# Optimization experiments

Measured on AMD Instinct MI355X. Metric: run time of the kernel, lower is better.

## Reference

```python
import jax, jax.numpy as jnp
import numpy as np

B, N, C, H = 4, 1024, 256, 8
HD = C // H
SCALE = HD ** -0.5


def setup_inputs() -> dict:
    key = jax.random.key(0)
    ks = jax.random.split(key, 8)
    x = jax.random.normal(ks[0], (B, N, C), jnp.float32)
    voxel_coord = jax.random.uniform(ks[1], (B, N, 3), jnp.float32)
    # Linear weights stored as [in, out] so y = x @ W + b (same math as torch x @ W.T)
    W_qk = jax.random.normal(ks[2], (C, 2 * C), jnp.float32) * 0.02
    W_v = jax.random.normal(ks[3], (C, C), jnp.float32) * 0.02
    W_proj = jax.random.normal(ks[4], (C, C), jnp.float32) * 0.02
    b_proj = jnp.zeros((C,), jnp.float32)
    W_pos = jax.random.normal(ks[5], (4, H), jnp.float32) * 0.02
    b_pos = jnp.zeros((H,), jnp.float32)
    gating = jnp.ones((H,), jnp.float32)
    return dict(x=x, voxel_coord=voxel_coord, W_qk=W_qk, W_v=W_v,
                W_proj=W_proj, b_proj=b_proj, W_pos=W_pos, b_pos=b_pos,
                gating=gating)


def reference(x, voxel_coord, W_qk, W_v, W_proj, b_proj, W_pos, b_pos, gating):
    b, n, c = x.shape
    # Relative 3D positional encoding: positions[b,i,j] = p[j] - p[i]; feature = [dx,dy,dz,dist]
    diff = voxel_coord[:, None, :, :] - voxel_coord[:, :, None, :]          # [B,N,N,3]
    dist = jnp.sqrt(jnp.sum(diff * diff, axis=-1, keepdims=True))           # [B,N,N,1]
    rel = jnp.concatenate([diff, dist], axis=-1)                            # [B,N,N,4]

    # Positional score per head, softmax over keys j
    pos_logits = jnp.einsum('bijf,fh->bhij', rel, W_pos) + b_pos[None, :, None, None]
    pos_score = jax.nn.softmax(pos_logits, axis=-1)                         # [B,H,N,N]

    # Content score: SDPA with V = I  ==  plain softmax attention matrix
    qk = (x @ W_qk).reshape(b, n, 2, H, HD)
    q = jnp.transpose(qk[:, :, 0], (0, 2, 1, 3))                            # [B,H,N,hd]
    k = jnp.transpose(qk[:, :, 1], (0, 2, 1, 3))
    patch_score = jax.nn.softmax(jnp.einsum('bhid,bhjd->bhij', q, k) * SCALE, axis=-1)

    # Gated mix + renormalize
    sig = jax.nn.sigmoid(gating)[None, :, None, None]
    attn = (1.0 - sig) * patch_score + sig * pos_score
    attn = attn / jnp.sum(attn, axis=-1, keepdims=True)

    v = (x @ W_v).reshape(b, n, H, HD).transpose(0, 2, 1, 3)                # [B,H,N,hd]
    out = jnp.einsum('bhij,bhjd->bihd', attn, v).reshape(b, n, c)           # [B,N,C]
    out = out @ W_proj + b_proj
    return out
```

## Files before the change

### kernel.cpp

```cpp
#include <hip/hip_runtime.h>
#include <hip/hip_bf16.h>

#define LOG2E 1.4426950408889634f

typedef __attribute__((ext_vector_type(8))) short bf16x8_t;
typedef __attribute__((ext_vector_type(4))) float f32x4_t;

#if __has_builtin(__builtin_amdgcn_exp2f)
#define EXP2F_(x) __builtin_amdgcn_exp2f(x)
#else
__device__ __forceinline__ float EXP2F_(float x) {
    float r; asm volatile("v_exp_f32 %0, %1\ns_nop 1" : "=v"(r) : "v"(x)); return r;
}
#endif
#if __has_builtin(__builtin_amdgcn_sqrtf)
#define SQRTF_(x) __builtin_amdgcn_sqrtf(x)
#else
__device__ __forceinline__ float SQRTF_(float x) {
    float r; asm volatile("v_sqrt_f32 %0, %1\ns_nop 1" : "=v"(r) : "v"(x)); return r;
}
#endif

__device__ __forceinline__ unsigned short f2bf(float f) {
    unsigned u = __float_as_uint(f);
    u += 0x7fffu + ((u >> 16) & 1u);
    return (unsigned short)(u >> 16);
}

__device__ __forceinline__ unsigned pk2(float lo, float hi) {
    union { __hip_bfloat162 h2; unsigned u; } cvt;
    cvt.h2 = __float22bfloat162_rn(make_float2(lo, hi));
    return cvt.u;
}

__device__ __forceinline__ void stage16(const unsigned short* g, unsigned short* l, int lane) {
#if __has_builtin(__builtin_amdgcn_global_load_lds)
    __builtin_amdgcn_global_load_lds((const __attribute__((address_space(1))) void*)g,
                                     (__attribute__((address_space(3))) void*)l, 16, 0, 0);
#else
    *(uint4*)((char*)l + lane * 16) = *(const uint4*)g;
#endif
}

__global__ __launch_bounds__(256) void k_convert(
    const float* __restrict__ x, const float* __restrict__ Wqk,
    const float* __restrict__ Wv, const float* __restrict__ Wpj,
    unsigned short* __restrict__ x_bf, unsigned short* __restrict__ Wqk_t,
    unsigned short* __restrict__ Wv_t, unsigned short* __restrict__ Wp_t)
{
    __shared__ unsigned short T[64 * 72];
    const int bid = blockIdx.x, tid = threadIdx.x;
    if (bid < 64) {
        const float* src; unsigned short* dst; int N_, kt, nt;
        if (bid < 32)      { src = Wqk; dst = Wqk_t; N_ = 512; kt = bid & 3; nt = bid >> 2; }
        else if (bid < 48) { int t = bid - 32; src = Wv;  dst = Wv_t; N_ = 256; kt = t & 3; nt = t >> 2; }
        else               { int t = bid - 48; src = Wpj; dst = Wp_t; N_ = 256; kt = t & 3; nt = t >> 2; }
        const int kr = tid >> 2, seg = tid & 3;
        #pragma unroll
        for (int u = 0; u < 4; ++u) {
            float4 v = *(const float4*)(src + (kt * 64 + kr) * N_ + nt * 64 + seg * 16 + u * 4);
            T[(seg * 16 + u * 4 + 0) * 72 + kr] = f2bf(v.x);
            T[(seg * 16 + u * 4 + 1) * 72 + kr] = f2bf(v.y);
            T[(seg * 16 + u * 4 + 2) * 72 + kr] = f2bf(v.z);
            T[(seg * 16 + u * 4 + 3) * 72 + kr] = f2bf(v.w);
        }
        __syncthreads();
        const int n = tid >> 2, s2 = tid & 3;
        uint4 a = *(uint4*)&T[n * 72 + s2 * 16];
        uint4 b2 = *(uint4*)&T[n * 72 + s2 * 16 + 8];
        *(uint4*)(dst + (nt * 64 + n) * 256 + kt * 64 + s2 * 16) = a;
        *(uint4*)(dst + (nt * 64 + n) * 256 + kt * 64 + s2 * 16 + 8) = b2;
    } else {
        const int cb2 = bid - 64;
        const float4* xs = (const float4*)x + (size_t)cb2 * 8192;
        uint2* xd = (uint2*)x_bf + (size_t)cb2 * 8192;
        for (int i = tid; i < 8192; i += 256) {
            float4 v = xs[i];
            uint2 o;
            o.x = (unsigned)f2bf(v.x) | ((unsigned)f2bf(v.y) << 16);
            o.y = (unsigned)f2bf(v.z) | ((unsigned)f2bf(v.w) << 16);
            xd[i] = o;
        }
    }
}

__global__ __launch_bounds__(256) void k_qkv(
    const unsigned short* __restrict__ x_bf,
    const unsigned short* __restrict__ Wqk_t,
    const unsigned short* __restrict__ Wv_t,
    unsigned short* __restrict__ q_ws, unsigned short* __restrict__ k_ws,
    unsigned short* __restrict__ v_ws)
{
    __shared__ unsigned short Al[64 * 64];
    __shared__ unsigned short Bl[64 * 64];
    const int tid = threadIdx.x;
    const int n0 = blockIdx.x * 64;
    const int row0 = blockIdx.y * 64;
    const int w = tid >> 6, lane = tid & 63;
    const int lhi = lane >> 4, llo = lane & 15;
    const unsigned short* Bsrc = (n0 < 512) ? (Wqk_t + n0 * 256) : (Wv_t + (n0 - 512) * 256);

    const int sr = lane >> 3, sc = lane & 7;
    const int scx = sc ^ (sr & 7);

    f32x4_t acc[4] = {};
    for (int kc = 0; kc < 4; ++kc) {
        #pragma unroll
        for (int s = 0; s < 2; ++s) {
            int chunk = w * 2 + s;
            int r = chunk * 8 + sr;
            stage16(x_bf + (row0 + r) * 256 + kc * 64 + scx * 8, &Al[chunk * 512], lane);
            stage16(Bsrc + r * 256 + kc * 64 + scx * 8, &Bl[chunk * 512], lane);
        }
        __syncthreads();
        #pragma unroll
        for (int ks = 0; ks < 2; ++ks) {
            int ua = ((ks * 4 + lhi) ^ (llo & 7)) * 8;
            bf16x8_t a = *(const bf16x8_t*)(&Al[(w * 16 + llo) * 64 + ua]);
            #pragma unroll
            for (int nt = 0; nt < 4; ++nt) {
                bf16x8_t b = *(const bf16x8_t*)(&Bl[(nt * 16 + llo) * 64 + ua]);
                acc[nt] = __builtin_amdgcn_mfma_f32_16x16x32_bf16(a, b, acc[nt], 0, 0, 0);
            }
        }
        __syncthreads();
    }
    constexpr float QSC = (float)(1.4426950408889634 / 5.656854249492380195206754896838);
    #pragma unroll
    for (int nt = 0; nt < 4; ++nt) {
        int ng = n0 + nt * 16 + llo;
        #pragma unroll
        for (int r = 0; r < 4; ++r) {
            int ig = row0 + w * 16 + lhi * 4 + r;
            float val = acc[nt][r];
            int b = ig >> 10, i = ig & 1023;
            if (ng < 256) {
                int h = ng >> 5, d = ng & 31;
                q_ws[((b * 8 + h) * 1024 + i) * 32 + d] = f2bf(val * QSC);
            } else if (ng < 512) {
                int c = ng - 256, h = c >> 5, d = c & 31;
                k_ws[((b * 8 + h) * 1024 + i) * 32 + d] = f2bf(val);
            } else {
                int c = ng - 512, h = c >> 5, d = c & 31;
                v_ws[((b * 8 + h) * 1024 + i) * 32 + d] = f2bf(val);
            }
        }
    }
}

__global__ __launch_bounds__(256) void k_attn(
    const unsigned short* __restrict__ q_ws,
    const unsigned short* __restrict__ k_ws,
    const unsigned short* __restrict__ v_ws,
    const float* __restrict__ coords,
    const float* __restrict__ W_pos,
    const float* __restrict__ b_pos,
    float* __restrict__ part)
{
    __shared__ unsigned short Kl[64 * 32];
    __shared__ unsigned short Vt[32 * 72];
    __shared__ unsigned short Wp[64 * 72];
    __shared__ unsigned short Wq[64 * 72];
    __shared__ float4 XYZS[512];
    __shared__ float  AJ[512];

    const int tid = threadIdx.x;
    const int bid = blockIdx.x;
    const int xcd = bid & 7, idx = bid >> 3;
    const int bh = xcd * 4 + (idx >> 5);
    const int rem = idx & 31;
    const int it = rem >> 1;
    const int jh = rem & 1;
    const int b = bh >> 3, h = bh & 7;

    const int w = tid >> 6, lane = tid & 63;
    const int lhi = lane >> 4, llo = lane & 15;

    const float wxl = W_pos[0 * 8 + h] * LOG2E;
    const float wyl = W_pos[1 * 8 + h] * LOG2E;
    const float wzl = W_pos[2 * 8 + h] * LOG2E;
    const float wdl = W_pos[3 * 8 + h] * LOG2E;
    const float bpl = b_pos[h] * LOG2E;

    const int i_base = it * 64 + w * 16;
    bf16x8_t qf = *(const bf16x8_t*)(q_ws + (bh * 1024 + i_base + llo) * 32 + lhi * 8);

    const float* cb_ = coords + b * 3072;
    const int ig = i_base + llo;
    float xi = cb_[ig * 3 + 0], yi = cb_[ig * 3 + 1], zi = cb_[ig * 3 + 2];
    float si = fmaf(xi, xi, fmaf(yi, yi, zi * zi));
    float cil = fmaf(wzl, zi, fmaf(wyl, yi, wxl * xi));

    for (int jl = tid; jl < 512; jl += 256) {
        int jg = jh * 512 + jl;
        float xj = cb_[jg * 3 + 0], yj = cb_[jg * 3 + 1], zj = cb_[jg * 3 + 2];
        XYZS[jl] = make_float4(xj, yj, zj, fmaf(xj, xj, fmaf(yj, yj, zj * zj)));
        AJ[jl] = fmaf(wzl, zj, fmaf(wyl, yj, wxl * xj)) + bpl;
    }

    bf16x8_t ones;
    #pragma unroll
    for (int e = 0; e < 8; ++e) ones[e] = (short)0x3F80;

    f32x4_t accP[2] = {}, accQ[2] = {};
    f32x4_t accLp = {}, accLq = {};

    const int ksr = lane >> 2, ksc = lane & 3;
    const int kscx = ksc ^ (ksr & 3);
    __syncthreads();

    for (int t = 0; t < 8; ++t) {
        const int j0 = jh * 512 + t * 64;
        const int jlb0 = t * 64;
        {
            int r = w * 16 + ksr;
            stage16(k_ws + (bh * 1024 + j0 + r) * 32 + kscx * 8, &Kl[w * 512], lane);
            uint4 vv = *(const uint4*)(v_ws + (bh * 1024 + j0 + lane) * 32 + w * 8);
            const unsigned short* pv = (const unsigned short*)&vv;
            #pragma unroll
            for (int e = 0; e < 8; ++e) Vt[(w * 8 + e) * 72 + lane] = pv[e];
        }
        __syncthreads();

        #pragma unroll
        for (int jq = 0; jq < 4; ++jq) {
            int krow = jq * 16 + llo;
            bf16x8_t kf = *(const bf16x8_t*)(&Kl[krow * 32 + ((lhi ^ (krow & 3)) * 8)]);
            f32x4_t zero = {};
            f32x4_t sv = __builtin_amdgcn_mfma_f32_16x16x32_bf16(kf, qf, zero, 0, 0, 0);
            int jlb = jlb0 + jq * 16 + lhi * 4;
            float ep[4], eq[4];
            #pragma unroll
            for (int r = 0; r < 4; ++r) {
                float4 cj = XYZS[jlb + r];
                float aj = AJ[jlb + r];
                float dot = fmaf(cj.x, xi, fmaf(cj.y, yi, cj.z * zi));
                float d2 = fmaf(-2.0f, dot, si + cj.w);
                float dist = SQRTF_(d2);
                float spos = fmaf(wdl, dist, aj - cil);
                ep[r] = EXP2F_(sv[r]);
                eq[r] = EXP2F_(spos);
            }
            uint2 wpP, wpQ;
            wpP.x = pk2(ep[0], ep[1]); wpP.y = pk2(ep[2], ep[3]);
            wpQ.x = pk2(eq[0], eq[1]); wpQ.y = pk2(eq[2], eq[3]);
            int off = (w * 16 + llo) * 72 + jq * 16 + lhi * 4;
            *(uint2*)(&Wp[off]) = wpP;
            *(uint2*)(&Wq[off]) = wpQ;
        }

        #pragma unroll
        for (int jb = 0; jb < 2; ++jb) {
            bf16x8_t bP = *(const bf16x8_t*)(&Wp[(w * 16 + llo) * 72 + jb * 32 + lhi * 8]);
            bf16x8_t bQ = *(const bf16x8_t*)(&Wq[(w * 16 + llo) * 72 + jb * 32 + lhi * 8]);
            accLp = __builtin_amdgcn_mfma_f32_16x16x32_bf16(ones, bP, accLp, 0, 0, 0);
            accLq = __builtin_amdgcn_mfma_f32_16x16x32_bf16(ones, bQ, accLq, 0, 0, 0);
            #pragma unroll
            for (int dt = 0; dt < 2; ++dt) {
                bf16x8_t af = *(const bf16x8_t*)(&Vt[(dt * 16 + llo) * 72 + jb * 32 + lhi * 8]);
                accP[dt] = __builtin_amdgcn_mfma_f32_16x16x32_bf16(af, bP, accP[dt], 0, 0, 0);
                accQ[dt] = __builtin_amdgcn_mfma_f32_16x16x32_bf16(af, bQ, accQ[dt], 0, 0, 0);
            }
        }
        __syncthreads();
    }

    float* pb = part + (size_t)((bh * 16 + it) * 2 + jh) * 4224;
    #pragma unroll
    for (int dt = 0; dt < 2; ++dt) {
        #pragma unroll
        for (int r = 0; r < 4; ++r) {
            int d = dt * 16 + lhi * 4 + r;
            pb[d * 64 + w * 16 + llo] = accP[dt][r];
            pb[2048 + d * 64 + w * 16 + llo] = accQ[dt][r];
        }
    }
    if (lane < 16) {
        pb[4096 + w * 16 + lane] = accLp[0];
        pb[4160 + w * 16 + lane] = accLq[0];
    }
}

__global__ __launch_bounds__(256) void k_comb(
    const float* __restrict__ part, const float* __restrict__ gating,
    unsigned short* __restrict__ o_ws)
{
    const int bid = blockIdx.x;
    const int bh = bid >> 4, it = bid & 15;
    const int b = bh >> 3, h = bh & 7;
    const int tid = threadIdx.x, w = tid >> 6, i = tid & 63;
    const float* p0 = part + (size_t)(bid * 2) * 4224;
    const float* p1 = p0 + 4224;
    float sig = 1.0f / (1.0f + __expf(-gating[h]));
    float Lp = p0[4096 + i] + p1[4096 + i];
    float Lq = p0[4160 + i] + p1[4160 + i];
    float ca = (1.0f - sig) / Lp, cb2 = sig / Lq;
    unsigned short ob[8];
    #pragma unroll
    for (int e = 0; e < 8; ++e) {
        int d = w * 8 + e;
        float Op = p0[d * 64 + i] + p1[d * 64 + i];
        float Oq = p0[2048 + d * 64 + i] + p1[2048 + d * 64 + i];
        ob[e] = f2bf(ca * Op + cb2 * Oq);
    }
    *(uint4*)(o_ws + ((size_t)(b * 1024 + it * 64 + i)) * 256 + h * 32 + w * 8) = *(uint4*)ob;
}

__global__ __launch_bounds__(256) void k_proj(
    const unsigned short* __restrict__ A,
    const unsigned short* __restrict__ Bt,
    const float* __restrict__ bias,
    float* __restrict__ out)
{
    __shared__ unsigned short Al[64 * 64];
    __shared__ unsigned short Bl[64 * 64];
    const int tid = threadIdx.x;
    const int n0 = blockIdx.x * 64;
    const int row0 = blockIdx.y * 64;
    const int w = tid >> 6, lane = tid & 63;
    const int lhi = lane >> 4, llo = lane & 15;
    const int sr = lane >> 3, sc = lane & 7;
    const int scx = sc ^ (sr & 7);

    f32x4_t acc[4] = {};
    for (int kc = 0; kc < 4; ++kc) {
        #pragma unroll
        for (int s = 0; s < 2; ++s) {
            int chunk = w * 2 + s;
            int r = chunk * 8 + sr;
            stage16(A + (row0 + r) * 256 + kc * 64 + scx * 8, &Al[chunk * 512], lane);
            stage16(Bt + (n0 + r) * 256 + kc * 64 + scx * 8, &Bl[chunk * 512], lane);
        }
        __syncthreads();
        #pragma unroll
        for (int ks = 0; ks < 2; ++ks) {
            int ua = ((ks * 4 + lhi) ^ (llo & 7)) * 8;
            bf16x8_t a = *(const bf16x8_t*)(&Al[(w * 16 + llo) * 64 + ua]);
            #pragma unroll
            for (int nt = 0; nt < 4; ++nt) {
                bf16x8_t b = *(const bf16x8_t*)(&Bl[(nt * 16 + llo) * 64 + ua]);
                acc[nt] = __builtin_amdgcn_mfma_f32_16x16x32_bf16(a, b, acc[nt], 0, 0, 0);
            }
        }
        __syncthreads();
    }
    #pragma unroll
    for (int nt = 0; nt < 4; ++nt) {
        int ng = n0 + nt * 16 + llo;
        float bv = bias[ng];
        #pragma unroll
        for (int r = 0; r < 4; ++r) {
            int ig = row0 + w * 16 + lhi * 4 + r;
            out[ig * 256 + ng] = acc[nt][r] + bv;
        }
    }
}

extern "C" void kernel_launch(void* const* d_in, const int* in_sizes, int n_in,
                              void* d_out, int out_size, void* d_ws, size_t ws_size,
                              hipStream_t stream)
{
    const float* x    = (const float*)d_in[0];
    const float* vc   = (const float*)d_in[1];
    const float* Wqk  = (const float*)d_in[2];
    const float* Wv   = (const float*)d_in[3];
    const float* Wpj  = (const float*)d_in[4];
    const float* bpj  = (const float*)d_in[5];
    const float* Wpos = (const float*)d_in[6];
    const float* bpos = (const float*)d_in[7];
    const float* gat  = (const float*)d_in[8];
    float* out = (float*)d_out;

    char* ws = (char*)d_ws;
    unsigned short* x_bf  = (unsigned short*)(ws + 0);
    unsigned short* Wqk_t = (unsigned short*)(ws + 2097152);
    unsigned short* Wv_t  = (unsigned short*)(ws + 2359296);
    unsigned short* Wp_t  = (unsigned short*)(ws + 2490368);
    unsigned short* q_ws  = (unsigned short*)(ws + 2621440);
    unsigned short* k_ws  = (unsigned short*)(ws + 4718592);
    unsigned short* v_ws  = (unsigned short*)(ws + 6815744);
    unsigned short* o_ws  = (unsigned short*)(ws + 8912896);
    float*          partf = (float*)(ws + 11010048);

    hipLaunchKernelGGL(k_convert, dim3(96), dim3(256), 0, stream,
                       x, Wqk, Wv, Wpj, x_bf, Wqk_t, Wv_t, Wp_t);
    hipLaunchKernelGGL(k_qkv, dim3(12, 64), dim3(256), 0, stream,
                       x_bf, Wqk_t, Wv_t, q_ws, k_ws, v_ws);
    hipLaunchKernelGGL(k_attn, dim3(1024), dim3(256), 0, stream,
                       q_ws, k_ws, v_ws, vc, Wpos, bpos, partf);
    hipLaunchKernelGGL(k_comb, dim3(512), dim3(256), 0, stream,
                       partf, gat, o_ws);
    hipLaunchKernelGGL(k_proj, dim3(4, 64), dim3(256), 0, stream,
                       o_ws, Wp_t, bpj, out);
}
```

Before: 125.7 us.

## Fuse combine into attention with in-block key split and convert x inside QKV GEMM

```diff
diff --git a/kernel.cpp b/kernel.cpp
--- a/kernel.cpp
+++ b/kernel.cpp
@@ -43,49 +43,36 @@
 }
 
 __global__ __launch_bounds__(256) void k_convert(
-    const float* __restrict__ x, const float* __restrict__ Wqk,
-    const float* __restrict__ Wv, const float* __restrict__ Wpj,
-    unsigned short* __restrict__ x_bf, unsigned short* __restrict__ Wqk_t,
-    unsigned short* __restrict__ Wv_t, unsigned short* __restrict__ Wp_t)
+    const float* __restrict__ Wqk, const float* __restrict__ Wv,
+    const float* __restrict__ Wpj,
+    unsigned short* __restrict__ Wqk_t, unsigned short* __restrict__ Wv_t,
+    unsigned short* __restrict__ Wp_t)
 {
     __shared__ unsigned short T[64 * 72];
     const int bid = blockIdx.x, tid = threadIdx.x;
-    if (bid < 64) {
-        const float* src; unsigned short* dst; int N_, kt, nt;
-        if (bid < 32)      { src = Wqk; dst = Wqk_t; N_ = 512; kt = bid & 3; nt = bid >> 2; }
-        else if (bid < 48) { int t = bid - 32; src = Wv;  dst = Wv_t; N_ = 256; kt = t & 3; nt = t >> 2; }
-        else               { int t = bid - 48; src = Wpj; dst = Wp_t; N_ = 256; kt = t & 3; nt = t >> 2; }
-        const int kr = tid >> 2, seg = tid & 3;
-        #pragma unroll
-        for (int u = 0; u < 4; ++u) {
-            float4 v = *(const float4*)(src + (kt * 64 + kr) * N_ + nt * 64 + seg * 16 + u * 4);
-            T[(seg * 16 + u * 4 + 0) * 72 + kr] = f2bf(v.x);
-            T[(seg * 16 + u * 4 + 1) * 72 + kr] = f2bf(v.y);
-            T[(seg * 16 + u * 4 + 2) * 72 + kr] = f2bf(v.z);
-            T[(seg * 16 + u * 4 + 3) * 72 + kr] = f2bf(v.w);
-        }
-        __syncthreads();
-        const int n = tid >> 2, s2 = tid & 3;
-        uint4 a = *(uint4*)&T[n * 72 + s2 * 16];
-        uint4 b2 = *(uint4*)&T[n * 72 + s2 * 16 + 8];
-        *(uint4*)(dst + (nt * 64 + n) * 256 + kt * 64 + s2 * 16) = a;
-        *(uint4*)(dst + (nt * 64 + n) * 256 + kt * 64 + s2 * 16 + 8) = b2;
-    } else {
-        const int cb2 = bid - 64;
-        const float4* xs = (const float4*)x + (size_t)cb2 * 8192;
-        uint2* xd = (uint2*)x_bf + (size_t)cb2 * 8192;
-        for (int i = tid; i < 8192; i += 256) {
-            float4 v = xs[i];
-            uint2 o;
-            o.x = (unsigned)f2bf(v.x) | ((unsigned)f2bf(v.y) << 16);
-            o.y = (unsigned)f2bf(v.z) | ((unsigned)f2bf(v.w) << 16);
-            xd[i] = o;
-        }
-    }
+    const float* src; unsigned short* dst; int N_, kt, nt;
+    if (bid < 32)      { src = Wqk; dst = Wqk_t; N_ = 512; kt = bid & 3; nt = bid >> 2; }
+    else if (bid < 48) { int t = bid - 32; src = Wv;  dst = Wv_t; N_ = 256; kt = t & 3; nt = t >> 2; }
+    else               { int t = bid - 48; src = Wpj; dst = Wp_t; N_ = 256; kt = t & 3; nt = t >> 2; }
+    const int kr = tid >> 2, seg = tid & 3;
+    #pragma unroll
+    for (int u = 0; u < 4; ++u) {
+        float4 v = *(const float4*)(src + (kt * 64 + kr) * N_ + nt * 64 + seg * 16 + u * 4);
+        T[(seg * 16 + u * 4 + 0) * 72 + kr] = f2bf(v.x);
+        T[(seg * 16 + u * 4 + 1) * 72 + kr] = f2bf(v.y);
+        T[(seg * 16 + u * 4 + 2) * 72 + kr] = f2bf(v.z);
+        T[(seg * 16 + u * 4 + 3) * 72 + kr] = f2bf(v.w);
+    }
+    __syncthreads();
+    const int n = tid >> 2, s2 = tid & 3;
+    uint4 a = *(uint4*)&T[n * 72 + s2 * 16];
+    uint4 b2 = *(uint4*)&T[n * 72 + s2 * 16 + 8];
+    *(uint4*)(dst + (nt * 64 + n) * 256 + kt * 64 + s2 * 16) = a;
+    *(uint4*)(dst + (nt * 64 + n) * 256 + kt * 64 + s2 * 16 + 8) = b2;
 }
 
 __global__ __launch_bounds__(256) void k_qkv(
-    const unsigned short* __restrict__ x_bf,
+    const float* __restrict__ x,
     const unsigned short* __restrict__ Wqk_t,
     const unsigned short* __restrict__ Wv_t,
     unsigned short* __restrict__ q_ws, unsigned short* __restrict__ k_ws,
@@ -101,7 +88,7 @@
     const unsigned short* Bsrc = (n0 < 512) ? (Wqk_t + n0 * 256) : (Wv_t + (n0 - 512) * 256);
 
     const int sr = lane >> 3, sc = lane & 7;
-    const int scx = sc ^ (sr & 7);
+    const int scx = sc ^ sr;
 
     f32x4_t acc[4] = {};
     for (int kc = 0; kc < 4; ++kc) {
@@ -109,7 +96,12 @@
         for (int s = 0; s < 2; ++s) {
             int chunk = w * 2 + s;
             int r = chunk * 8 + sr;
-            stage16(x_bf + (row0 + r) * 256 + kc * 64 + scx * 8, &Al[chunk * 512], lane);
+            const float* ax = x + (row0 + r) * 256 + kc * 64 + scx * 8;
+            float4 a0 = *(const float4*)ax, a1 = *(const float4*)(ax + 4);
+            uint4 pk;
+            pk.x = pk2(a0.x, a0.y); pk.y = pk2(a0.z, a0.w);
+            pk.z = pk2(a1.x, a1.y); pk.w = pk2(a1.z, a1.w);
+            *(uint4*)(&Al[r * 64 + sc * 8]) = pk;
             stage16(Bsrc + r * 256 + kc * 64 + scx * 8, &Bl[chunk * 512], lane);
         }
         __syncthreads();
@@ -148,32 +140,32 @@
     }
 }
 
-__global__ __launch_bounds__(256) void k_attn(
+__global__ __launch_bounds__(512, 6) void k_attn(
     const unsigned short* __restrict__ q_ws,
     const unsigned short* __restrict__ k_ws,
     const unsigned short* __restrict__ v_ws,
     const float* __restrict__ coords,
     const float* __restrict__ W_pos,
     const float* __restrict__ b_pos,
-    float* __restrict__ part)
-{
-    __shared__ unsigned short Kl[64 * 32];
-    __shared__ unsigned short Vt[32 * 72];
-    __shared__ unsigned short Wp[64 * 72];
-    __shared__ unsigned short Wq[64 * 72];
-    __shared__ float4 XYZS[512];
-    __shared__ float  AJ[512];
+    const float* __restrict__ gating,
+    unsigned short* __restrict__ o_ws)
+{
+    __shared__ unsigned short Kl[2 * 64 * 32];
+    __shared__ unsigned short Vt[2 * 32 * 64];
+    __shared__ unsigned short Wp[2 * 64 * 64];
+    __shared__ unsigned short Wq[2 * 64 * 64];
+    __shared__ float4 TX[128];
+    __shared__ float  TA[128];
 
     const int tid = threadIdx.x;
     const int bid = blockIdx.x;
-    const int xcd = bid & 7, idx = bid >> 3;
-    const int bh = xcd * 4 + (idx >> 5);
-    const int rem = idx & 31;
-    const int it = rem >> 1;
-    const int jh = rem & 1;
+    const int xcd = bid & 7, s = bid >> 3;
+    const int bh = xcd * 4 + (s >> 4);
+    const int it = s & 15;
     const int b = bh >> 3, h = bh & 7;
 
     const int w = tid >> 6, lane = tid & 63;
+    const int wi = w & 3, wj = w >> 2;
     const int lhi = lane >> 4, llo = lane & 15;
 
     const float wxl = W_pos[0 * 8 + h] * LOG2E;
@@ -182,7 +174,7 @@
     const float wdl = W_pos[3 * 8 + h] * LOG2E;
     const float bpl = b_pos[h] * LOG2E;
 
-    const int i_base = it * 64 + w * 16;
+    const int i_base = it * 64 + wi * 16;
     bf16x8_t qf = *(const bf16x8_t*)(q_ws + (bh * 1024 + i_base + llo) * 32 + lhi * 8);
 
     const float* cb_ = coords + b * 3072;
@@ -191,13 +183,6 @@
     float si = fmaf(xi, xi, fmaf(yi, yi, zi * zi));
     float cil = fmaf(wzl, zi, fmaf(wyl, yi, wxl * xi));
 
-    for (int jl = tid; jl < 512; jl += 256) {
-        int jg = jh * 512 + jl;
-        float xj = cb_[jg * 3 + 0], yj = cb_[jg * 3 + 1], zj = cb_[jg * 3 + 2];
-        XYZS[jl] = make_float4(xj, yj, zj, fmaf(xj, xj, fmaf(yj, yj, zj * zj)));
-        AJ[jl] = fmaf(wzl, zj, fmaf(wyl, yj, wxl * xj)) + bpl;
-    }
-
     bf16x8_t ones;
     #pragma unroll
     for (int e = 0; e < 8; ++e) ones[e] = (short)0x3F80;
@@ -205,35 +190,40 @@
     f32x4_t accP[2] = {}, accQ[2] = {};
     f32x4_t accLp = {}, accLq = {};
 
-    const int ksr = lane >> 2, ksc = lane & 3;
-    const int kscx = ksc ^ (ksr & 3);
-    __syncthreads();
+    const int jhbase = wj * 512;
+    const int wc = w & 3;
 
     for (int t = 0; t < 8; ++t) {
-        const int j0 = jh * 512 + t * 64;
-        const int jlb0 = t * 64;
+        const int j0s = (w >> 2) * 512 + t * 64;
+        stage16(k_ws + (bh * 1024 + j0s + wc * 16 + (lane >> 2)) * 32 + (lane & 3) * 8,
+                &Kl[(w >> 2) * 2048 + wc * 512], lane);
         {
-            int r = w * 16 + ksr;
-            stage16(k_ws + (bh * 1024 + j0 + r) * 32 + kscx * 8, &Kl[w * 512], lane);
-            uint4 vv = *(const uint4*)(v_ws + (bh * 1024 + j0 + lane) * 32 + w * 8);
+            uint4 vv = *(const uint4*)(v_ws + (bh * 1024 + j0s + lane) * 32 + wc * 8);
             const unsigned short* pv = (const unsigned short*)&vv;
             #pragma unroll
-            for (int e = 0; e < 8; ++e) Vt[(w * 8 + e) * 72 + lane] = pv[e];
+            for (int e = 0; e < 8; ++e)
+                Vt[((w >> 2) * 32 + wc * 8 + e) * 64 + (((lane >> 3) ^ e) * 8) + (lane & 7)] = pv[e];
+        }
+        if (tid < 128) {
+            int half = tid >> 6, jl = tid & 63;
+            int jg = half * 512 + t * 64 + jl;
+            float xj = cb_[jg * 3 + 0], yj = cb_[jg * 3 + 1], zj = cb_[jg * 3 + 2];
+            TX[half * 64 + jl] = make_float4(xj, yj, zj, fmaf(xj, xj, fmaf(yj, yj, zj * zj)));
+            TA[half * 64 + jl] = fmaf(wzl, zj, fmaf(wyl, yj, wxl * xj)) + bpl;
         }
         __syncthreads();
 
         #pragma unroll
         for (int jq = 0; jq < 4; ++jq) {
-            int krow = jq * 16 + llo;
-            bf16x8_t kf = *(const bf16x8_t*)(&Kl[krow * 32 + ((lhi ^ (krow & 3)) * 8)]);
+            bf16x8_t kf = *(const bf16x8_t*)(&Kl[wj * 2048 + (jq * 16 + llo) * 32 + lhi * 8]);
             f32x4_t zero = {};
             f32x4_t sv = __builtin_amdgcn_mfma_f32_16x16x32_bf16(kf, qf, zero, 0, 0, 0);
-            int jlb = jlb0 + jq * 16 + lhi * 4;
+            int jlb = wj * 64 + jq * 16 + lhi * 4;
             float ep[4], eq[4];
             #pragma unroll
             for (int r = 0; r < 4; ++r) {
-                float4 cj = XYZS[jlb + r];
-                float aj = AJ[jlb + r];
+                float4 cj = TX[jlb + r];
+                float aj = TA[jlb + r];
                 float dot = fmaf(cj.x, xi, fmaf(cj.y, yi, cj.z * zi));
                 float d2 = fmaf(-2.0f, dot, si + cj.w);
                 float dist = SQRTF_(d2);
@@ -241,23 +231,25 @@
                 ep[r] = EXP2F_(sv[r]);
                 eq[r] = EXP2F_(spos);
             }
-            uint2 wpP, wpQ;
-            wpP.x = pk2(ep[0], ep[1]); wpP.y = pk2(ep[2], ep[3]);
-            wpQ.x = pk2(eq[0], eq[1]); wpQ.y = pk2(eq[2], eq[3]);
-            int off = (w * 16 + llo) * 72 + jq * 16 + lhi * 4;
-            *(uint2*)(&Wp[off]) = wpP;
-            *(uint2*)(&Wq[off]) = wpQ;
+            int row = wj * 64 + wi * 16 + llo;
+            int off = row * 64 + (((jq * 2 + (lhi >> 1)) ^ (llo & 7)) * 8) + (lhi & 1) * 4;
+            uint2 uP, uQ;
+            uP.x = pk2(ep[0], ep[1]); uP.y = pk2(ep[2], ep[3]);
+            uQ.x = pk2(eq[0], eq[1]); uQ.y = pk2(eq[2], eq[3]);
+            *(uint2*)(&Wp[off]) = uP;
+            *(uint2*)(&Wq[off]) = uQ;
         }
 
         #pragma unroll
         for (int jb = 0; jb < 2; ++jb) {
-            bf16x8_t bP = *(const bf16x8_t*)(&Wp[(w * 16 + llo) * 72 + jb * 32 + lhi * 8]);
-            bf16x8_t bQ = *(const bf16x8_t*)(&Wq[(w * 16 + llo) * 72 + jb * 32 + lhi * 8]);
+            int uu = ((jb * 4 + lhi) ^ (llo & 7)) * 8;
+            bf16x8_t bP = *(const bf16x8_t*)(&Wp[(wj * 64 + wi * 16 + llo) * 64 + uu]);
+            bf16x8_t bQ = *(const bf16x8_t*)(&Wq[(wj * 64 + wi * 16 + llo) * 64 + uu]);
             accLp = __builtin_amdgcn_mfma_f32_16x16x32_bf16(ones, bP, accLp, 0, 0, 0);
             accLq = __builtin_amdgcn_mfma_f32_16x16x32_bf16(ones, bQ, accLq, 0, 0, 0);
             #pragma unroll
             for (int dt = 0; dt < 2; ++dt) {
-                bf16x8_t af = *(const bf16x8_t*)(&Vt[(dt * 16 + llo) * 72 + jb * 32 + lhi * 8]);
+                bf16x8_t af = *(const bf16x8_t*)(&Vt[(wj * 32 + dt * 16 + llo) * 64 + uu]);
                 accP[dt] = __builtin_amdgcn_mfma_f32_16x16x32_bf16(af, bP, accP[dt], 0, 0, 0);
                 accQ[dt] = __builtin_amdgcn_mfma_f32_16x16x32_bf16(af, bQ, accQ[dt], 0, 0, 0);
             }
@@ -265,45 +257,33 @@
         __syncthreads();
     }
 
-    float* pb = part + (size_t)((bh * 16 + it) * 2 + jh) * 4224;
-    #pragma unroll
-    for (int dt = 0; dt < 2; ++dt) {
-        #pragma unroll
-        for (int r = 0; r < 4; ++r) {
-            int d = dt * 16 + lhi * 4 + r;
-            pb[d * 64 + w * 16 + llo] = accP[dt][r];
-            pb[2048 + d * 64 + w * 16 + llo] = accQ[dt][r];
-        }
-    }
-    if (lane < 16) {
-        pb[4096 + w * 16 + lane] = accLp[0];
-        pb[4160 + w * 16 + lane] = accLq[0];
-    }
-}
-
-__global__ __launch_bounds__(256) void k_comb(
-    const float* __restrict__ part, const float* __restrict__ gating,
-    unsigned short* __restrict__ o_ws)
-{
-    const int bid = blockIdx.x;
-    const int bh = bid >> 4, it = bid & 15;
-    const int b = bh >> 3, h = bh & 7;
-    const int tid = threadIdx.x, w = tid >> 6, i = tid & 63;
-    const float* p0 = part + (size_t)(bid * 2) * 4224;
-    const float* p1 = p0 + 4224;
-    float sig = 1.0f / (1.0f + __expf(-gating[h]));
-    float Lp = p0[4096 + i] + p1[4096 + i];
-    float Lq = p0[4160 + i] + p1[4160 + i];
-    float ca = (1.0f - sig) / Lp, cb2 = sig / Lq;
-    unsigned short ob[8];
-    #pragma unroll
-    for (int e = 0; e < 8; ++e) {
-        int d = w * 8 + e;
-        float Op = p0[d * 64 + i] + p1[d * 64 + i];
-        float Oq = p0[2048 + d * 64 + i] + p1[2048 + d * 64 + i];
-        ob[e] = f2bf(ca * Op + cb2 * Oq);
-    }
-    *(uint4*)(o_ws + ((size_t)(b * 1024 + it * 64 + i)) * 256 + h * 32 + w * 8) = *(uint4*)ob;
+    float* red = (float*)Wp;
+    float* LPQ = (float*)Wq;
+    if (wj == 1) {
+        float* pr = red + (wi * 64 + lane) * 16;
+        *(f32x4_t*)(pr + 0) = accP[0]; *(f32x4_t*)(pr + 4)  = accP[1];
+        *(f32x4_t*)(pr + 8) = accQ[0]; *(f32x4_t*)(pr + 12) = accQ[1];
+        if (lhi == 0) { LPQ[wi * 16 + llo] = accLp[0]; LPQ[64 + wi * 16 + llo] = accLq[0]; }
+    }
+    __syncthreads();
+    if (wj == 0) {
+        const float* pr = red + (wi * 64 + lane) * 16;
+        float Lp = accLp[0] + LPQ[wi * 16 + llo];
+        float Lq = accLq[0] + LPQ[64 + wi * 16 + llo];
+        float sig = 1.0f / (1.0f + __expf(-gating[h]));
+        float ca = (1.0f - sig) / Lp, cb2 = sig / Lq;
+        int rowg = b * 1024 + it * 64 + wi * 16 + llo;
+        #pragma unroll
+        for (int dt = 0; dt < 2; ++dt) {
+            float o0 = ca * (accP[dt][0] + pr[dt * 4 + 0]) + cb2 * (accQ[dt][0] + pr[8 + dt * 4 + 0]);
+            float o1 = ca * (accP[dt][1] + pr[dt * 4 + 1]) + cb2 * (accQ[dt][1] + pr[8 + dt * 4 + 1]);
+            float o2 = ca * (accP[dt][2] + pr[dt * 4 + 2]) + cb2 * (accQ[dt][2] + pr[8 + dt * 4 + 2]);
+            float o3 = ca * (accP[dt][3] + pr[dt * 4 + 3]) + cb2 * (accQ[dt][3] + pr[8 + dt * 4 + 3]);
+            uint2 uu;
+            uu.x = pk2(o0, o1); uu.y = pk2(o2, o3);
+            *(uint2*)(o_ws + (size_t)rowg * 256 + h * 32 + dt * 16 + lhi * 4) = uu;
+        }
+    }
 }
 
 __global__ __launch_bounds__(256) void k_proj(
@@ -320,7 +300,7 @@
     const int w = tid >> 6, lane = tid & 63;
     const int lhi = lane >> 4, llo = lane & 15;
     const int sr = lane >> 3, sc = lane & 7;
-    const int scx = sc ^ (sr & 7);
+    const int scx = sc ^ sr;
 
     f32x4_t acc[4] = {};
     for (int kc = 0; kc < 4; ++kc) {
@@ -372,24 +352,20 @@
     float* out = (float*)d_out;
 
     char* ws = (char*)d_ws;
-    unsigned short* x_bf  = (unsigned short*)(ws + 0);
-    unsigned short* Wqk_t = (unsigned short*)(ws + 2097152);
-    unsigned short* Wv_t  = (unsigned short*)(ws + 2359296);
-    unsigned short* Wp_t  = (unsigned short*)(ws + 2490368);
-    unsigned short* q_ws  = (unsigned short*)(ws + 2621440);
-    unsigned short* k_ws  = (unsigned short*)(ws + 4718592);
-    unsigned short* v_ws  = (unsigned short*)(ws + 6815744);
-    unsigned short* o_ws  = (unsigned short*)(ws + 8912896);
-    float*          partf = (float*)(ws + 11010048);
-
-    hipLaunchKernelGGL(k_convert, dim3(96), dim3(256), 0, stream,
-                       x, Wqk, Wv, Wpj, x_bf, Wqk_t, Wv_t, Wp_t);
+    unsigned short* Wqk_t = (unsigned short*)(ws + 0);
+    unsigned short* Wv_t  = (unsigned short*)(ws + 262144);
+    unsigned short* Wp_t  = (unsigned short*)(ws + 393216);
+    unsigned short* q_ws  = (unsigned short*)(ws + 524288);
+    unsigned short* k_ws  = (unsigned short*)(ws + 2621440);
+    unsigned short* v_ws  = (unsigned short*)(ws + 4718592);
+    unsigned short* o_ws  = (unsigned short*)(ws + 6815744);
+
+    hipLaunchKernelGGL(k_convert, dim3(64), dim3(256), 0, stream,
+                       Wqk, Wv, Wpj, Wqk_t, Wv_t, Wp_t);
     hipLaunchKernelGGL(k_qkv, dim3(12, 64), dim3(256), 0, stream,
-                       x_bf, Wqk_t, Wv_t, q_ws, k_ws, v_ws);
-    hipLaunchKernelGGL(k_attn, dim3(1024), dim3(256), 0, stream,
-                       q_ws, k_ws, v_ws, vc, Wpos, bpos, partf);
-    hipLaunchKernelGGL(k_comb, dim3(512), dim3(256), 0, stream,
-                       partf, gat, o_ws);
+                       x, Wqk_t, Wv_t, q_ws, k_ws, v_ws);
+    hipLaunchKernelGGL(k_attn, dim3(512), dim3(512), 0, stream,
+                       q_ws, k_ws, v_ws, vc, Wpos, bpos, gat, o_ws);
     hipLaunchKernelGGL(k_proj, dim3(4, 64), dim3(256), 0, stream,
                        o_ws, Wp_t, bpj, out);
 }
```

Measured after the change: 123.7 us. Within noise of the previous version (-1.6%).
